# Optimization experiments

Measured on AMD Instinct MI355X. Metric: run time of the kernel, lower is better.

Reference implementation:

```python
import jax, jax.numpy as jnp
import numpy as np

B, S, D_IN, D_OUT = 4, 8192, 1024, 1024


def setup_inputs() -> dict:
    key = jax.random.key(0)
    k1, k2, k3, k4 = jax.random.split(key, 4)
    x = jax.random.normal(k1, (B, S, D_IN), dtype=jnp.float32)
    # signed int8 weights, stored int8 as in the torch buffer
    weight_int = jax.random.randint(k2, (D_OUT, D_IN), -128, 128, dtype=jnp.int32).astype(jnp.int8)
    # realistic per-output-channel scales
    weight_scale = jax.random.uniform(k3, (D_OUT,), dtype=jnp.float32, minval=0.005, maxval=0.02)
    input_scale = jnp.asarray(0.05, dtype=jnp.float32)
    bias = jax.random.normal(k4, (D_OUT,), dtype=jnp.float32) * 0.01
    return {"x": x, "weight_int": weight_int, "weight_scale": weight_scale,
            "input_scale": input_scale, "bias": bias}


def reference(x, weight_int, weight_scale, input_scale, bias):
    # quantize activations to int8 (faithful: round, clamp, cast)
    x_int = jnp.clip(jnp.round(x / input_scale), -128, 127).astype(jnp.int8)
    # module upcasts both operands to fp32 for the matmul
    out = jnp.matmul(x_int.astype(jnp.float32), weight_int.astype(jnp.float32).T)
    # dequantize: per-output-channel weight scale * scalar input scale, then bias
    out = out * weight_scale * input_scale + bias
    return out
```

## Files before the change

### kernel.cpp

```cpp
#include <hip/hip_runtime.h>
#include <stdint.h>
#include <stddef.h>

typedef int   v4i __attribute__((ext_vector_type(4)));
typedef float v4f __attribute__((ext_vector_type(4)));

#define M_DIM 32768
#define N_DIM 1024
#define K_DIM 1024
#define BM 64
#define KSTEPS 16

__global__ __launch_bounds__(256)
void repack_w_kernel(const int* __restrict__ w32, int* __restrict__ wf)
{
    const int i  = blockIdx.x * 256 + threadIdx.x;
    const int f  = i >> 8;
    const int r  = i & 255;
    const int ln = r >> 2;
    const int dw = r & 3;
    const int j  = f & 3;
    const int ks = (f >> 2) & 15;
    const int wv = (f >> 6) & 7;
    const int np = f >> 9;
    const int n  = np * 512 + wv * 64 + j * 16 + (ln & 15);
    const int k  = ks * 64 + (ln >> 4) * 16 + dw * 4;
    const v4i v  = *(const v4i*)&w32[(size_t)n * K_DIM + k];
    wf[i] = (v[0] & 255) | ((v[1] & 255) << 8) |
            ((v[2] & 255) << 16) | ((v[3] & 255) << 24);
}

__global__ __launch_bounds__(512, 4)
void fused_kernel(const float* __restrict__ x,
                  const signed char* __restrict__ Wf,
                  const float* __restrict__ wscale,
                  const float* __restrict__ iscale_p,
                  const float* __restrict__ bias,
                  float* __restrict__ out)
{
    __shared__ signed char lA[BM * K_DIM];

    const int mrow0 = blockIdx.x * BM;
    const int t  = threadIdx.x;
    const int wv = t >> 6;
    const int ln = t & 63;
    const int lr = ln & 15;
    const int kh = (ln >> 4) * 16;

    {
        const float inv = 1.0f / *iscale_p;
        const int colf = (t & 255) * 4;
        const int rsub = t >> 8;
        for (int jb = 0; jb < 4; ++jb) {
            v4f vv[8];
            #pragma unroll
            for (int u = 0; u < 8; ++u) {
                const int row = (jb * 8 + u) * 2 + rsub;
                vv[u] = *(const v4f*)&x[(size_t)(mrow0 + row) * K_DIM + colf];
            }
            #pragma unroll
            for (int u = 0; u < 8; ++u) {
                const int row = (jb * 8 + u) * 2 + rsub;
                int r = 0;
                #pragma unroll
                for (int e = 0; e < 4; ++e) {
                    float q = rintf(vv[u][e] * inv);
                    q = fminf(127.f, fmaxf(-128.f, q));
                    r |= ((int)q & 255) << (8 * e);
                }
                *(int*)&lA[row * K_DIM + (colf ^ ((row & 7) << 4))] = r;
            }
        }
    }
    __syncthreads();

    const float is = *iscale_p;

    for (int np = 0; np < 2; ++np) {
        v4i acc[4][4] = {};
        #pragma unroll 4
        for (int ks = 0; ks < KSTEPS; ++ks) {
            v4i aF[4], bF[4];
            #pragma unroll
            for (int i = 0; i < 4; ++i) {
                const int row = i * 16 + lr;
                aF[i] = *(const v4i*)&lA[row * K_DIM +
                                         ((ks * 64 + kh) ^ ((row & 7) << 4))];
            }
            const size_t fbase = ((size_t)(np * 8 + wv) * 16 + ks) * 4;
            #pragma unroll
            for (int j = 0; j < 4; ++j)
                bF[j] = *(const v4i*)&Wf[(fbase + j) * 1024 + ln * 16];
            #pragma unroll
            for (int i = 0; i < 4; ++i)
                #pragma unroll
                for (int j = 0; j < 4; ++j)
                    acc[i][j] = __builtin_amdgcn_mfma_i32_16x16x64_i8(
                                    bF[j], aF[i], acc[i][j], 0, 0, 0);
        }
        #pragma unroll
        for (int j = 0; j < 4; ++j) {
            const int nb = np * 512 + wv * 64 + j * 16 + ((ln >> 4) << 2);
            v4f sc4 = *(const v4f*)&wscale[nb];
            const v4f bv4 = *(const v4f*)&bias[nb];
            sc4 *= is;
            #pragma unroll
            for (int i = 0; i < 4; ++i) {
                const int m = mrow0 + i * 16 + lr;
                v4f o;
                #pragma unroll
                for (int r = 0; r < 4; ++r)
                    o[r] = (float)acc[i][j][r] * sc4[r] + bv4[r];
                *(v4f*)&out[(size_t)m * N_DIM + nb] = o;
            }
        }
    }
}

extern "C" void kernel_launch(void* const* d_in, const int* in_sizes, int n_in,
                              void* d_out, int out_size, void* d_ws, size_t ws_size,
                              hipStream_t stream)
{
    const float* x       = (const float*)d_in[0];
    const int*   w32     = (const int*)d_in[1];
    const float* wscale  = (const float*)d_in[2];
    const float* iscale  = (const float*)d_in[3];
    const float* bias    = (const float*)d_in[4];
    float* out           = (float*)d_out;

    signed char* wf = (signed char*)d_ws;

    repack_w_kernel<<<(N_DIM * K_DIM / 4) / 256, 256, 0, stream>>>(w32, (int*)wf);

    fused_kernel<<<M_DIM / BM, 512, 0, stream>>>(x, wf, wscale, iscale, bias, out);
}
```

Before: 74.72 us.

## Overlap activation quantization with first N-pass MFMA and split N into quarters

Instead of quantizing the whole 64x1024 activation tile before any compute, each k-step prefetches and quantizes the next 64-column slab while the MFMAs for the current slab run. This hides global x loads behind the first N-pass. N is split into four 256-wide passes with a 4x2 accumulator tile, which cuts accumulator registers, and the weight repack layout is changed to match. The LDS swizzle gains an extra bit to reduce bank conflicts. The cost is a __syncthreads per k-step in the first pass and three more passes that each reread the A tile from LDS.

```diff
diff --git a/kernel.cpp b/kernel.cpp
--- a/kernel.cpp
+++ b/kernel.cpp
@@ -2,6 +2,7 @@
 #include <stdint.h>
 #include <stddef.h>
 
+typedef int   v2i __attribute__((ext_vector_type(2)));
 typedef int   v4i __attribute__((ext_vector_type(4)));
 typedef float v4f __attribute__((ext_vector_type(4)));
 
@@ -11,6 +12,10 @@
 #define BM 64
 #define KSTEPS 16
 
+__device__ __forceinline__ int swzS(int row) {
+    return ((row & 7) << 4) ^ ((row & 1) << 6);
+}
+
 __global__ __launch_bounds__(256)
 void repack_w_kernel(const int* __restrict__ w32, int* __restrict__ wf)
 {
@@ -19,11 +24,11 @@
     const int r  = i & 255;
     const int ln = r >> 2;
     const int dw = r & 3;
-    const int j  = f & 3;
-    const int ks = (f >> 2) & 15;
-    const int wv = (f >> 6) & 7;
-    const int np = f >> 9;
-    const int n  = np * 512 + wv * 64 + j * 16 + (ln & 15);
+    const int j  = f & 1;
+    const int ks = (f >> 1) & 15;
+    const int wv = (f >> 5) & 7;
+    const int p  = f >> 8;
+    const int n  = p * 256 + wv * 32 + j * 16 + (ln & 15);
     const int k  = ks * 64 + (ln >> 4) * 16 + dw * 4;
     const v4i v  = *(const v4i*)&w32[(size_t)n * K_DIM + k];
     wf[i] = (v[0] & 255) | ((v[1] & 255) << 8) |
@@ -46,61 +51,75 @@
     const int ln = t & 63;
     const int lr = ln & 15;
     const int kh = (ln >> 4) * 16;
+    const float inv = 1.0f / *iscale_p;
+    const float is  = *iscale_p;
+
+    const int qrow = t >> 3;
+    const int qc   = (t & 7) * 8;
+    const float* xrow = &x[(size_t)(mrow0 + qrow) * K_DIM];
+    signed char* lArow = &lA[qrow * K_DIM];
+    const int qs = swzS(qrow);
+
+    #define PACK8(A_, B_, PR_)                                              \
+        do {                                                                 \
+            int lo_ = 0, hi_ = 0;                                            \
+            _Pragma("unroll")                                                \
+            for (int e_ = 0; e_ < 4; ++e_) {                                 \
+                float qa_ = rintf((A_)[e_] * inv);                           \
+                qa_ = fminf(127.f, fmaxf(-128.f, qa_));                      \
+                lo_ |= ((int)qa_ & 255) << (8 * e_);                         \
+                float qb_ = rintf((B_)[e_] * inv);                           \
+                qb_ = fminf(127.f, fmaxf(-128.f, qb_));                      \
+                hi_ |= ((int)qb_ & 255) << (8 * e_);                         \
+            }                                                                \
+            (PR_)[0] = lo_; (PR_)[1] = hi_;                                  \
+        } while (0)
 
     {
-        const float inv = 1.0f / *iscale_p;
-        const int colf = (t & 255) * 4;
-        const int rsub = t >> 8;
-        for (int jb = 0; jb < 4; ++jb) {
-            v4f vv[8];
-            #pragma unroll
-            for (int u = 0; u < 8; ++u) {
-                const int row = (jb * 8 + u) * 2 + rsub;
-                vv[u] = *(const v4f*)&x[(size_t)(mrow0 + row) * K_DIM + colf];
-            }
-            #pragma unroll
-            for (int u = 0; u < 8; ++u) {
-                const int row = (jb * 8 + u) * 2 + rsub;
-                int r = 0;
-                #pragma unroll
-                for (int e = 0; e < 4; ++e) {
-                    float q = rintf(vv[u][e] * inv);
-                    q = fminf(127.f, fmaxf(-128.f, q));
-                    r |= ((int)q & 255) << (8 * e);
-                }
-                *(int*)&lA[row * K_DIM + (colf ^ ((row & 7) << 4))] = r;
-            }
-        }
+        const v4f a = *(const v4f*)&xrow[qc];
+        const v4f b = *(const v4f*)&xrow[qc + 4];
+        v2i pr;
+        PACK8(a, b, pr);
+        *(v2i*)&lArow[qc ^ qs] = pr;
     }
     __syncthreads();
 
-    const float is = *iscale_p;
-
-    for (int np = 0; np < 2; ++np) {
-        v4i acc[4][4] = {};
-        #pragma unroll 4
+    {
+        v4i acc[4][2] = {};
         for (int ks = 0; ks < KSTEPS; ++ks) {
-            v4i aF[4], bF[4];
+            const bool pf = (ks + 1 < KSTEPS);
+            v4f xa, xb;
+            if (pf) {
+                xa = *(const v4f*)&xrow[(ks + 1) * 64 + qc];
+                xb = *(const v4f*)&xrow[(ks + 1) * 64 + qc + 4];
+            }
+            v4i bF[2];
+            const size_t fb = ((size_t)wv * 16 + ks) * 2;
+            bF[0] = *(const v4i*)&Wf[fb * 1024 + ln * 16];
+            bF[1] = *(const v4i*)&Wf[(fb + 1) * 1024 + ln * 16];
+            v4i aF[4];
             #pragma unroll
             for (int i = 0; i < 4; ++i) {
                 const int row = i * 16 + lr;
                 aF[i] = *(const v4i*)&lA[row * K_DIM +
-                                         ((ks * 64 + kh) ^ ((row & 7) << 4))];
+                                         ((ks * 64 + kh) ^ swzS(row))];
             }
-            const size_t fbase = ((size_t)(np * 8 + wv) * 16 + ks) * 4;
-            #pragma unroll
-            for (int j = 0; j < 4; ++j)
-                bF[j] = *(const v4i*)&Wf[(fbase + j) * 1024 + ln * 16];
             #pragma unroll
             for (int i = 0; i < 4; ++i)
                 #pragma unroll
-                for (int j = 0; j < 4; ++j)
+                for (int j = 0; j < 2; ++j)
                     acc[i][j] = __builtin_amdgcn_mfma_i32_16x16x64_i8(
                                     bF[j], aF[i], acc[i][j], 0, 0, 0);
+            if (pf) {
+                v2i pr;
+                PACK8(xa, xb, pr);
+                *(v2i*)&lArow[(((ks + 1) * 64) + qc) ^ qs] = pr;
+                __syncthreads();
+            }
         }
         #pragma unroll
-        for (int j = 0; j < 4; ++j) {
-            const int nb = np * 512 + wv * 64 + j * 16 + ((ln >> 4) << 2);
+        for (int j = 0; j < 2; ++j) {
+            const int nb = wv * 32 + j * 16 + ((ln >> 4) << 2);
             v4f sc4 = *(const v4f*)&wscale[nb];
             const v4f bv4 = *(const v4f*)&bias[nb];
             sc4 *= is;
@@ -115,6 +134,47 @@
             }
         }
     }
+
+    for (int p = 1; p < 4; ++p) {
+        v4i acc[4][2] = {};
+        #pragma unroll 4
+        for (int ks = 0; ks < KSTEPS; ++ks) {
+            v4i bF[2];
+            const size_t fb = ((size_t)(p * 8 + wv) * 16 + ks) * 2;
+            bF[0] = *(const v4i*)&Wf[fb * 1024 + ln * 16];
+            bF[1] = *(const v4i*)&Wf[(fb + 1) * 1024 + ln * 16];
+            v4i aF[4];
+            #pragma unroll
+            for (int i = 0; i < 4; ++i) {
+                const int row = i * 16 + lr;
+                aF[i] = *(const v4i*)&lA[row * K_DIM +
+                                         ((ks * 64 + kh) ^ swzS(row))];
+            }
+            #pragma unroll
+            for (int i = 0; i < 4; ++i)
+                #pragma unroll
+                for (int j = 0; j < 2; ++j)
+                    acc[i][j] = __builtin_amdgcn_mfma_i32_16x16x64_i8(
+                                    bF[j], aF[i], acc[i][j], 0, 0, 0);
+        }
+        #pragma unroll
+        for (int j = 0; j < 2; ++j) {
+            const int nb = p * 256 + wv * 32 + j * 16 + ((ln >> 4) << 2);
+            v4f sc4 = *(const v4f*)&wscale[nb];
+            const v4f bv4 = *(const v4f*)&bias[nb];
+            sc4 *= is;
+            #pragma unroll
+            for (int i = 0; i < 4; ++i) {
+                const int m = mrow0 + i * 16 + lr;
+                v4f o;
+                #pragma unroll
+                for (int r = 0; r < 4; ++r)
+                    o[r] = (float)acc[i][j][r] * sc4[r] + bv4[r];
+                *(v4f*)&out[(size_t)m * N_DIM + nb] = o;
+            }
+        }
+    }
+    #undef PACK8
 }
 
 extern "C" void kernel_launch(void* const* d_in, const int* in_sizes, int n_in,
```

After: 71.08 us. 4.9% less time.
